# Optimization experiments

Measured on AMD Instinct MI355X. Metric: run time of the kernel, lower is better.

## Reference

```python
import jax, jax.numpy as jnp
import numpy as np

N_S = 50000
N_T = 50000
N = N_S + N_T
D = 128
NEG_SLOPE = 0.2


def gat_conv(x, src, dst, W, a_src, a_dst, n_nodes):
    """PyG GATConv, heads=1, bias=False, add_self_loops=True (loops already appended by caller? no: here)."""
    h = x @ W.T                                   # [N, out]
    loops = jnp.arange(n_nodes, dtype=src.dtype)
    src = jnp.concatenate([src, loops])
    dst = jnp.concatenate([dst, loops])
    a_s = h @ a_src                               # [N]
    a_d = h @ a_dst                               # [N]
    e = jax.nn.leaky_relu(a_s[src] + a_d[dst], NEG_SLOPE)   # [E]
    e_max = jax.ops.segment_max(e, dst, num_segments=n_nodes)
    e = jnp.exp(e - e_max[dst])
    denom = jax.ops.segment_sum(e, dst, num_segments=n_nodes)
    alpha = e / (denom[dst] + 1e-16)
    out = jax.ops.segment_sum(h[src] * alpha[:, None], dst, num_segments=n_nodes)
    return out


def setup_inputs() -> dict:
    key = jax.random.key(0)
    ks = jax.random.split(key, 16)
    E = 500000
    edge_index = jax.random.randint(ks[0], (2, E), 0, N_S, dtype=jnp.int64)
    paper_edge_index = jax.random.randint(ks[1], (2, E), 0, N, dtype=jnp.int64)
    author_edge_index = jax.random.randint(ks[2], (2, E), 0, N, dtype=jnp.int64)
    x_s = jax.random.normal(ks[3], (N_S, D), dtype=jnp.float32)
    x_t = jax.random.normal(ks[4], (N_T, D), dtype=jnp.float32)
    s = 1.0 / np.sqrt(D)
    return {
        "edge_index": edge_index,
        "paper_edge_index": paper_edge_index,
        "author_edge_index": author_edge_index,
        "x_s": x_s,
        "x_t": x_t,
        "Ws": jax.random.normal(ks[5], (D, D), dtype=jnp.float32) * s,
        "bs": jax.random.normal(ks[6], (D,), dtype=jnp.float32) * s,
        "Wt": jax.random.normal(ks[7], (D, D), dtype=jnp.float32) * s,
        "bt": jax.random.normal(ks[8], (D,), dtype=jnp.float32) * s,
        "W1": jax.random.normal(ks[9], (D, D), dtype=jnp.float32) * s,
        "a1s": jax.random.normal(ks[10], (D,), dtype=jnp.float32) * s,
        "a1d": jax.random.normal(ks[11], (D,), dtype=jnp.float32) * s,
        "W2": jax.random.normal(ks[12], (D, D), dtype=jnp.float32) * s,
        "a2s": jax.random.normal(ks[13], (D,), dtype=jnp.float32) * s,
        "a2d": jax.random.normal(ks[14], (D,), dtype=jnp.float32) * s,
    }


def reference(edge_index, paper_edge_index, author_edge_index, x_s, x_t,
              Ws, bs, Wt, bt, W1, a1s, a1d, W2, a2s, a2d):
    # training=None -> no dropout
    x_s = x_s @ Ws.T + bs
    x_t = x_t @ Wt.T + bt
    src = edge_index[0]
    dst = edge_index[1] + N_S  # reindex target nodes into concatenated space
    x = jnp.concatenate([x_s, x_t], axis=0)  # [N, D]

    # conv_1: bipartite edges s->t plus author-author edges
    src1 = jnp.concatenate([src, author_edge_index[0]])
    dst1 = jnp.concatenate([dst, author_edge_index[1]])
    new_x_t = jax.nn.relu(gat_conv(x, src1, dst1, W1, a1s, a1d, N))

    # conv_2: transposed bipartite edges t->s plus paper-paper edges
    src2 = jnp.concatenate([dst, paper_edge_index[0]])
    dst2 = jnp.concatenate([src, paper_edge_index[1]])
    new_x_s = jax.nn.relu(gat_conv(x, src2, dst2, W2, a2s, a2d, N))

    return (new_x_s[:N_S], new_x_t[N_S:])
```

## Files before the change

kernel.cpp:

```cpp
#include <hip/hip_runtime.h>
#include <hip/hip_bf16.h>

#define E0   500000
#define NS   50000
#define DD   128
#define ETOT (2*E0 + NS)

#define OFF_H1   0UL
#define OFF_H2   6400000UL
#define OFF_AS1  12800000UL
#define OFF_AD1  12900000UL
#define OFF_AS2  13000000UL
#define OFF_AD2  13100000UL
#define OFF_DEG1 13200000UL
#define OFF_DEG2 13250000UL
#define OFF_RP1  13300000UL
#define OFF_RP2  13351000UL
#define OFF_CUR1 13402000UL
#define OFF_CUR2 13452000UL
#define OFF_PS   13502000UL
#define OFF_PREF 13502128UL
#define OFF_REC1 13502256UL
#define OFF_REC2 15702256UL

typedef __bf16 bf16x8 __attribute__((ext_vector_type(8)));
typedef float f32x4 __attribute__((ext_vector_type(4)));

__device__ __forceinline__ ushort f2bf(float f) {
    uint b = __float_as_uint(f);
    return (ushort)((b + 0x7FFFu + ((b >> 16) & 1u)) >> 16);
}
__device__ __forceinline__ float bf2f(ushort u) { return __uint_as_float(((uint)u) << 16); }
__device__ __forceinline__ uint pk2(float a, float b) {
    return (uint)f2bf(a) | ((uint)f2bf(b) << 16);
}

__device__ __forceinline__ void stage_w_bf16(ushort* Wl, const float* __restrict__ W, int tid) {
#pragma unroll
    for (int i = 0; i < 8; i++) {
        const int idx = i * 256 + tid;
        const int row = idx >> 4, ch = idx & 15;
        const float4 f0 = *(const float4*)(W + row * DD + ch * 8);
        const float4 f1 = *(const float4*)(W + row * DD + ch * 8 + 4);
        uint4 v = make_uint4(pk2(f0.x, f0.y), pk2(f0.z, f0.w), pk2(f1.x, f1.y), pk2(f1.z, f1.w));
        *(uint4*)((char*)Wl + ((row * 256 + ch * 16) ^ ((row & 7) << 4))) = v;
    }
}

__device__ __forceinline__ void stage_x(ushort* Xl, const float* __restrict__ xin,
                                        int row0, int tid) {
#pragma unroll
    for (int i = 0; i < 4; i++) {
        const int idx = i * 256 + tid;
        const int r = idx >> 4, ch = idx & 15;
        const int gr = row0 + r;
        float4 f0 = make_float4(0.f, 0.f, 0.f, 0.f), f1 = f0;
        if (gr < NS) {
            f0 = *(const float4*)(xin + (size_t)gr * DD + ch * 8);
            f1 = *(const float4*)(xin + (size_t)gr * DD + ch * 8 + 4);
        }
        uint4 v = make_uint4(pk2(f0.x, f0.y), pk2(f0.z, f0.w), pk2(f1.x, f1.y), pk2(f1.z, f1.w));
        *(uint4*)((char*)Xl + ((r * 256 + ch * 16) ^ ((r & 7) << 4))) = v;
    }
}

__device__ __forceinline__ void mfma_phase(const ushort* Wl, const ushort* Xl,
                                           int wrow, int lane, f32x4 acc[8]) {
    const int l15 = lane & 15, q = lane >> 4;
    bf16x8 a[4];
#pragma unroll
    for (int ks = 0; ks < 4; ks++) {
        const int row = wrow + l15;
        const int byte = (row * 256 + (ks * 32 + q * 8) * 2) ^ ((row & 7) << 4);
        a[ks] = *(const bf16x8*)((const char*)Xl + byte);
    }
#pragma unroll
    for (int nt = 0; nt < 8; nt++) {
        const int n = nt * 16 + l15;
#pragma unroll
        for (int ks = 0; ks < 4; ks++) {
            const int byte = (n * 256 + (ks * 32 + q * 8) * 2) ^ ((n & 7) << 4);
            bf16x8 b = *(const bf16x8*)((const char*)Wl + byte);
            acc[nt] = __builtin_amdgcn_mfma_f32_16x16x32_bf16(a[ks], b, acc[nt], 0, 0, 0);
        }
    }
}

__device__ __forceinline__ void epi23(const f32x4 acc[8], int half, int row0, int wrow,
                                      int lane, const float* __restrict__ avs,
                                      const float* __restrict__ avd,
                                      ushort* __restrict__ h,
                                      float* __restrict__ as_, float* __restrict__ ad_) {
    const int l15 = lane & 15, q = lane >> 4;
    float vs[8], vd[8];
#pragma unroll
    for (int nt = 0; nt < 8; nt++) { vs[nt] = avs[nt * 16 + l15]; vd[nt] = avd[nt * 16 + l15]; }
#pragma unroll
    for (int r = 0; r < 4; r++) {
        const int gr = row0 + wrow + q * 4 + r;
        const bool ok = gr < NS;
        const size_t node = (size_t)(half * NS + gr);
        float ps = 0.f, pd = 0.f;
#pragma unroll
        for (int nt = 0; nt < 8; nt++) {
            const float v = acc[nt][r];
            ps += v * vs[nt];
            pd += v * vd[nt];
            if (ok) h[node * DD + nt * 16 + l15] = f2bf(v);
        }
#pragma unroll
        for (int m = 8; m; m >>= 1) { ps += __shfl_xor(ps, m); pd += __shfl_xor(pd, m); }
        if (ok && l15 == 0) { as_[node] = ps; ad_[node] = pd; }
    }
}

__global__ __launch_bounds__(256) void k_gemm(
    const float* __restrict__ xs, const float* __restrict__ xt,
    const float* __restrict__ Ws, const float* __restrict__ bs,
    const float* __restrict__ Wt, const float* __restrict__ bt,
    const float* __restrict__ W1, const float* __restrict__ a1s, const float* __restrict__ a1d,
    const float* __restrict__ W2, const float* __restrict__ a2s, const float* __restrict__ a2d,
    ushort* __restrict__ h1, ushort* __restrict__ h2,
    float* __restrict__ as1, float* __restrict__ ad1,
    float* __restrict__ as2, float* __restrict__ ad2) {
    __shared__ __align__(16) ushort Wl[128 * 128];
    __shared__ __align__(16) ushort Xl[64 * 128];
    const int tid = threadIdx.x;
    const int lane = tid & 63, wv = tid >> 6, wrow = wv * 16;
    const int l15 = lane & 15, q = lane >> 4;
    const int half = blockIdx.y;
    const int row0 = blockIdx.x * 64;
    const float* xin = half ? xt : xs;
    const float* W0  = half ? Wt : Ws;
    const float* b0  = half ? bt : bs;

    stage_w_bf16(Wl, W0, tid);
    stage_x(Xl, xin, row0, tid);
    __syncthreads();

    f32x4 acc[8];
#pragma unroll
    for (int nt = 0; nt < 8; nt++) acc[nt] = 0.f;
    mfma_phase(Wl, Xl, wrow, lane, acc);

#pragma unroll
    for (int nt = 0; nt < 8; nt++) {
        const float bvv = b0[nt * 16 + l15];
#pragma unroll
        for (int r = 0; r < 4; r++) {
            const int row = wrow + q * 4 + r;
            const int byte = (row * 256 + (nt * 16 + l15) * 2) ^ ((row & 7) << 4);
            *(ushort*)((char*)Xl + byte) = f2bf(acc[nt][r] + bvv);
        }
    }
    __syncthreads();
    stage_w_bf16(Wl, W1, tid);
    __syncthreads();

#pragma unroll
    for (int nt = 0; nt < 8; nt++) acc[nt] = 0.f;
    mfma_phase(Wl, Xl, wrow, lane, acc);
    epi23(acc, half, row0, wrow, lane, a1s, a1d, h1, as1, ad1);

    __syncthreads();
    stage_w_bf16(Wl, W2, tid);
    __syncthreads();

#pragma unroll
    for (int nt = 0; nt < 8; nt++) acc[nt] = 0.f;
    mfma_phase(Wl, Xl, wrow, lane, acc);
    epi23(acc, half, row0, wrow, lane, a2s, a2d, h2, as2, ad2);
}

__global__ void k_count_both(const int* __restrict__ ei, const int* __restrict__ pei,
                             const int* __restrict__ aei,
                             int* __restrict__ deg1, int* __restrict__ deg2) {
    const int e = blockIdx.x * 256 + threadIdx.x;
    if (e >= ETOT) return;
    if (e < E0) {
        const int a = ei[e], b = ei[E0 + e];
        atomicAdd(&deg1[b], 1);
        atomicAdd(&deg2[a], 1);
    } else if (e < 2 * E0) {
        const int k = e - E0;
        const int d1 = aei[E0 + k];
        if (d1 >= NS) atomicAdd(&deg1[d1 - NS], 1);
        const int d2 = pei[E0 + k];
        if (d2 < NS) atomicAdd(&deg2[d2], 1);
    } else {
        const int k = e - 2 * E0;
        atomicAdd(&deg1[k], 1);
        atomicAdd(&deg2[k], 1);
    }
}

__device__ __forceinline__ int wave_incl_scan(int x, int lane) {
#pragma unroll
    for (int off = 1; off < 64; off <<= 1) {
        const int v = __shfl_up(x, off);
        if (lane >= off) x += v;
    }
    return x;
}

__device__ __forceinline__ int4 load_deg4(const int* __restrict__ d, int idx) {
    if (idx + 3 < NS) return *(const int4*)(d + idx);
    int4 v = make_int4(0, 0, 0, 0);
    if (idx + 0 < NS) v.x = d[idx + 0];
    if (idx + 1 < NS) v.y = d[idx + 1];
    if (idx + 2 < NS) v.z = d[idx + 2];
    if (idx + 3 < NS) v.w = d[idx + 3];
    return v;
}

__global__ __launch_bounds__(256) void k_scan1(const int* __restrict__ deg,
                                               int* __restrict__ psum) {
    const int conv = blockIdx.y, blk = blockIdx.x, t = threadIdx.x;
    const int* d = deg + conv * NS;
    const int4 v = load_deg4(d, blk * 1024 + t * 4);
    int s = v.x + v.y + v.z + v.w;
#pragma unroll
    for (int m = 32; m; m >>= 1) s += __shfl_xor(s, m);
    __shared__ int wsum[4];
    const int lane = t & 63, wv = t >> 6;
    if (lane == 0) wsum[wv] = s;
    __syncthreads();
    if (t == 0) psum[conv * 64 + blk] = wsum[0] + wsum[1] + wsum[2] + wsum[3];
}

__global__ __launch_bounds__(128) void k_scan2(const int* __restrict__ psum,
                                               int* __restrict__ pref) {
    const int t = threadIdx.x;
    const int w = t >> 6, lane = t & 63;
    const int x = (lane < 49) ? psum[w * 64 + lane] : 0;
    const int incl = wave_incl_scan(x, lane);
    if (lane < 49) pref[w * 64 + lane] = incl - x;
}

__global__ __launch_bounds__(256) void k_scan3(const int* __restrict__ deg,
                                               const int* __restrict__ pref,
                                               int* __restrict__ rp1, int* __restrict__ cur1,
                                               int* __restrict__ rp2, int* __restrict__ cur2) {
    const int conv = blockIdx.y, blk = blockIdx.x, t = threadIdx.x;
    const int* d = deg + conv * NS;
    int* rp  = conv ? rp2  : rp1;
    int* cur = conv ? cur2 : cur1;
    const int idx = blk * 1024 + t * 4;
    const int4 v = load_deg4(d, idx);
    const int tsum = v.x + v.y + v.z + v.w;
    const int lane = t & 63, wv = t >> 6;
    const int incl = wave_incl_scan(tsum, lane);
    __shared__ int wsum[4];
    if (lane == 63) wsum[wv] = incl;
    __syncthreads();
    int woff = 0;
#pragma unroll
    for (int i = 0; i < 4; i++) woff += (i < wv) ? wsum[i] : 0;
    int ex = pref[conv * 64 + blk] + woff + (incl - tsum);
    if (idx + 0 < NS) { rp[idx + 0] = ex; cur[idx + 0] = ex; } ex += v.x;
    if (idx + 1 < NS) { rp[idx + 1] = ex; cur[idx + 1] = ex; } ex += v.y;
    if (idx + 2 < NS) { rp[idx + 2] = ex; cur[idx + 2] = ex; } ex += v.z;
    if (idx + 3 < NS) { rp[idx + 3] = ex; cur[idx + 3] = ex; } ex += v.w;
    if (blk == 48 && t == 0)
        rp[NS] = pref[conv * 64 + 48] + wsum[0] + wsum[1] + wsum[2] + wsum[3];
}

__device__ __forceinline__ float att_ee(float as_v, float ad_v) {
    float v = as_v + ad_v;
    v = v > 0.f ? v : 0.2f * v;
    return __expf(v);
}

__global__ void k_fill_both(const int* __restrict__ ei, const int* __restrict__ pei,
                            const int* __restrict__ aei,
                            const float* __restrict__ as1, const float* __restrict__ ad1,
                            const float* __restrict__ as2, const float* __restrict__ ad2,
                            int* __restrict__ cur1, float2* __restrict__ rec1,
                            int* __restrict__ cur2, float2* __restrict__ rec2) {
    const int e = blockIdx.x * 256 + threadIdx.x;
    if (e >= ETOT) return;
    if (e < E0) {
        const int a = ei[e], b = ei[E0 + e];
        {
            const float ee = att_ee(as1[a], ad1[b + NS]);
            const int pos = atomicAdd(&cur1[b], 1);
            rec1[pos] = make_float2(__int_as_float(a), ee);
        }
        {
            const float ee = att_ee(as2[b + NS], ad2[a]);
            const int pos = atomicAdd(&cur2[a], 1);
            rec2[pos] = make_float2(__int_as_float(b + NS), ee);
        }
    } else if (e < 2 * E0) {
        const int k = e - E0;
        const int s1 = aei[k], d1 = aei[E0 + k];
        if (d1 >= NS) {
            const float ee = att_ee(as1[s1], ad1[d1]);
            const int pos = atomicAdd(&cur1[d1 - NS], 1);
            rec1[pos] = make_float2(__int_as_float(s1), ee);
        }
        const int s2 = pei[k], d2 = pei[E0 + k];
        if (d2 < NS) {
            const float ee = att_ee(as2[s2], ad2[d2]);
            const int pos = atomicAdd(&cur2[d2], 1);
            rec2[pos] = make_float2(__int_as_float(s2), ee);
        }
    } else {
        const int k = e - 2 * E0;
        {
            const float ee = att_ee(as1[NS + k], ad1[NS + k]);
            const int pos = atomicAdd(&cur1[k], 1);
            rec1[pos] = make_float2(__int_as_float(NS + k), ee);
        }
        {
            const float ee = att_ee(as2[k], ad2[k]);
            const int pos = atomicAdd(&cur2[k], 1);
            rec2[pos] = make_float2(__int_as_float(k), ee);
        }
    }
}

__device__ __forceinline__ void fma8(float acc[8], float e, const uint4 q) {
    acc[0] += e * __uint_as_float(q.x << 16);
    acc[1] += e * __uint_as_float(q.x & 0xFFFF0000u);
    acc[2] += e * __uint_as_float(q.y << 16);
    acc[3] += e * __uint_as_float(q.y & 0xFFFF0000u);
    acc[4] += e * __uint_as_float(q.z << 16);
    acc[5] += e * __uint_as_float(q.z & 0xFFFF0000u);
    acc[6] += e * __uint_as_float(q.w << 16);
    acc[7] += e * __uint_as_float(q.w & 0xFFFF0000u);
}

__global__ __launch_bounds__(256) void k_gather(
    const int* __restrict__ rp1, const float2* __restrict__ rec1, const ushort* __restrict__ h1,
    const int* __restrict__ rp2, const float2* __restrict__ rec2, const ushort* __restrict__ h2,
    float* __restrict__ out) {
    const int conv = blockIdx.y;
    const int* rp = conv ? rp2 : rp1;
    const float2* rec = conv ? rec2 : rec1;
    const ushort* h = conv ? h2 : h1;
    float* outb = conv ? out : out + (size_t)NS * DD;
    const int node = blockIdx.x * 4 + (threadIdx.x >> 6);
    const int lane = threadIdx.x & 63;
    const int g = lane >> 4, l16 = lane & 15;
    const int beg = rp[node], end = rp[node + 1];
    float acc[8];
#pragma unroll
    for (int i = 0; i < 8; i++) acc[i] = 0.f;
    float es = 0.f;

    for (int e = beg + g * 4; e < end; e += 16) {
        float w[4];
        int s[4];
#pragma unroll
        for (int u = 0; u < 4; u++) {
            const bool ok = (e + u < end);
            const float2 r = ok ? rec[e + u] : make_float2(0.f, 0.f);
            s[u] = ok ? __float_as_int(r.x) : 0;
            w[u] = r.y;
        }
        uint4 q[4];
#pragma unroll
        for (int u = 0; u < 4; u++)
            q[u] = *(const uint4*)(h + (size_t)s[u] * DD + l16 * 8);
#pragma unroll
        for (int u = 0; u < 4; u++) {
            es += w[u];
            fma8(acc, w[u], q[u]);
        }
    }

#pragma unroll
    for (int i = 0; i < 8; i++) {
        acc[i] += __shfl_xor(acc[i], 16);
        acc[i] += __shfl_xor(acc[i], 32);
    }
    es += __shfl_xor(es, 16);
    es += __shfl_xor(es, 32);

    if (g == 0) {
        const float inv = 1.f / (es + 1e-16f);
        float4 o0, o1;
        o0.x = fmaxf(acc[0] * inv, 0.f);
        o0.y = fmaxf(acc[1] * inv, 0.f);
        o0.z = fmaxf(acc[2] * inv, 0.f);
        o0.w = fmaxf(acc[3] * inv, 0.f);
        o1.x = fmaxf(acc[4] * inv, 0.f);
        o1.y = fmaxf(acc[5] * inv, 0.f);
        o1.z = fmaxf(acc[6] * inv, 0.f);
        o1.w = fmaxf(acc[7] * inv, 0.f);
        *(float4*)(outb + (size_t)node * DD + l16 * 8) = o0;
        *(float4*)(outb + (size_t)node * DD + l16 * 8 + 4) = o1;
    }
}

extern "C" void kernel_launch(void* const* d_in, const int* in_sizes, int n_in,
                              void* d_out, int out_size, void* d_ws, size_t ws_size,
                              hipStream_t stream) {
    const int* ei  = (const int*)d_in[0];
    const int* pei = (const int*)d_in[1];
    const int* aei = (const int*)d_in[2];
    const float* xs  = (const float*)d_in[3];
    const float* xt  = (const float*)d_in[4];
    const float* Ws  = (const float*)d_in[5];
    const float* bs  = (const float*)d_in[6];
    const float* Wt  = (const float*)d_in[7];
    const float* bt  = (const float*)d_in[8];
    const float* W1  = (const float*)d_in[9];
    const float* a1s = (const float*)d_in[10];
    const float* a1d = (const float*)d_in[11];
    const float* W2  = (const float*)d_in[12];
    const float* a2s = (const float*)d_in[13];
    const float* a2d = (const float*)d_in[14];
    float* ws  = (float*)d_ws;
    float* out = (float*)d_out;

    ushort* h1 = (ushort*)(ws + OFF_H1);
    ushort* h2 = (ushort*)(ws + OFF_H2);
    int* deg1 = (int*)(ws + OFF_DEG1);
    int* rp1  = (int*)(ws + OFF_RP1);
    int* rp2  = (int*)(ws + OFF_RP2);
    int* cur1 = (int*)(ws + OFF_CUR1);
    int* cur2 = (int*)(ws + OFF_CUR2);
    int* psum = (int*)(ws + OFF_PS);
    int* pref = (int*)(ws + OFF_PREF);
    float2* rec1 = (float2*)(ws + OFF_REC1);
    float2* rec2 = (float2*)(ws + OFF_REC2);

    hipMemsetAsync(deg1, 0, 2 * NS * sizeof(int), stream);

    k_gemm<<<dim3((NS + 63) / 64, 2), 256, 0, stream>>>(
        xs, xt, Ws, bs, Wt, bt, W1, a1s, a1d, W2, a2s, a2d,
        h1, h2, ws + OFF_AS1, ws + OFF_AD1, ws + OFF_AS2, ws + OFF_AD2);

    const int eb = (ETOT + 255) / 256;
    k_count_both<<<eb, 256, 0, stream>>>(ei, pei, aei, deg1, deg1 + NS);
    k_scan1<<<dim3(49, 2), 256, 0, stream>>>(deg1, psum);
    k_scan2<<<1, 128, 0, stream>>>(psum, pref);
    k_scan3<<<dim3(49, 2), 256, 0, stream>>>(deg1, pref, rp1, cur1, rp2, cur2);
    k_fill_both<<<eb, 256, 0, stream>>>(ei, pei, aei,
                                        ws + OFF_AS1, ws + OFF_AD1, ws + OFF_AS2, ws + OFF_AD2,
                                        cur1, rec1, cur2, rec2);
    k_gather<<<dim3(NS / 4, 2), 256, 0, stream>>>(rp1, rec1, h1, rp2, rec2, h2, out);
}
```

Measured before the change: 366.5 us.

## Record atomic slots at count time and fuse CSR fill into GEMM launch

The degree-count pass now stores each edge's atomic slot, so the CSR fill becomes a plain scatter with no second round of atomics and no cursor arrays. That scatter is merged into the GEMM kernel as extra blocks, letting memory-bound edge work overlap the MFMA-bound projection blocks in a single launch. The per-edge attention exponent moves into the gather kernel, computed from as/ad lookups, so records shrink to 4-byte source indices. The cost is an extra slot array written and read, one more random as[] load per edge inside the gather, and a fused kernel whose edge blocks are forced to the GEMM block's shared-memory and launch-bounds footprint.

```diff
diff --git a/kernel.cpp b/kernel.cpp
--- a/kernel.cpp
+++ b/kernel.cpp
@@ -6,22 +6,25 @@
 #define DD   128
 #define ETOT (2*E0 + NS)
 
-#define OFF_H1   0UL
-#define OFF_H2   6400000UL
-#define OFF_AS1  12800000UL
-#define OFF_AD1  12900000UL
-#define OFF_AS2  13000000UL
-#define OFF_AD2  13100000UL
-#define OFF_DEG1 13200000UL
-#define OFF_DEG2 13250000UL
-#define OFF_RP1  13300000UL
-#define OFF_RP2  13351000UL
-#define OFF_CUR1 13402000UL
-#define OFF_CUR2 13452000UL
-#define OFF_PS   13502000UL
-#define OFF_PREF 13502128UL
-#define OFF_REC1 13502256UL
-#define OFF_REC2 15702256UL
+#define GEMM_BLOCKS 1564
+#define EDGE_BLOCKS 4102
+
+#define OFF_H1    0UL
+#define OFF_H2    6400000UL
+#define OFF_AS1   12800000UL
+#define OFF_AD1   12900000UL
+#define OFF_AS2   13000000UL
+#define OFF_AD2   13100000UL
+#define OFF_DEG1  13200000UL
+#define OFF_DEG2  13250000UL
+#define OFF_RP1   13300000UL
+#define OFF_RP2   13351000UL
+#define OFF_PS    13402000UL
+#define OFF_PREF  13402128UL
+#define OFF_SLOT1 13402256UL
+#define OFF_SLOT2 14452256UL
+#define OFF_REC1  15502256UL
+#define OFF_REC2  16552256UL
 
 typedef __bf16 bf16x8 __attribute__((ext_vector_type(8)));
 typedef float f32x4 __attribute__((ext_vector_type(4)));
@@ -30,7 +33,6 @@
     uint b = __float_as_uint(f);
     return (ushort)((b + 0x7FFFu + ((b >> 16) & 1u)) >> 16);
 }
-__device__ __forceinline__ float bf2f(ushort u) { return __uint_as_float(((uint)u) << 16); }
 __device__ __forceinline__ uint pk2(float a, float b) {
     return (uint)f2bf(a) | ((uint)f2bf(b) << 16);
 }
@@ -114,7 +116,7 @@
     }
 }
 
-__global__ __launch_bounds__(256) void k_gemm(
+__global__ __launch_bounds__(256) void k_fat(
     const float* __restrict__ xs, const float* __restrict__ xt,
     const float* __restrict__ Ws, const float* __restrict__ bs,
     const float* __restrict__ Wt, const float* __restrict__ bt,
@@ -122,14 +124,41 @@
     const float* __restrict__ W2, const float* __restrict__ a2s, const float* __restrict__ a2d,
     ushort* __restrict__ h1, ushort* __restrict__ h2,
     float* __restrict__ as1, float* __restrict__ ad1,
-    float* __restrict__ as2, float* __restrict__ ad2) {
+    float* __restrict__ as2, float* __restrict__ ad2,
+    const int* __restrict__ ei, const int* __restrict__ pei, const int* __restrict__ aei,
+    const int* __restrict__ rp1, const int* __restrict__ rp2,
+    const int* __restrict__ slot1, const int* __restrict__ slot2,
+    int* __restrict__ rec1, int* __restrict__ rec2) {
     __shared__ __align__(16) ushort Wl[128 * 128];
     __shared__ __align__(16) ushort Xl[64 * 128];
+    const int bid = blockIdx.x;
     const int tid = threadIdx.x;
+
+    if (bid >= GEMM_BLOCKS) {
+        const int e = (bid - GEMM_BLOCKS) * 256 + tid;
+        if (e >= ETOT) return;
+        if (e < E0) {
+            const int a = ei[e], b = ei[E0 + e];
+            rec1[rp1[b] + slot1[e]] = a;
+            rec2[rp2[a] + slot2[e]] = b + NS;
+        } else if (e < 2 * E0) {
+            const int k = e - E0;
+            const int s1 = aei[k], d1 = aei[E0 + k];
+            if (d1 >= NS) rec1[rp1[d1 - NS] + slot1[e]] = s1;
+            const int s2 = pei[k], d2 = pei[E0 + k];
+            if (d2 < NS) rec2[rp2[d2] + slot2[e]] = s2;
+        } else {
+            const int k = e - 2 * E0;
+            rec1[rp1[k] + slot1[e]] = NS + k;
+            rec2[rp2[k] + slot2[e]] = k;
+        }
+        return;
+    }
+
     const int lane = tid & 63, wv = tid >> 6, wrow = wv * 16;
     const int l15 = lane & 15, q = lane >> 4;
-    const int half = blockIdx.y;
-    const int row0 = blockIdx.x * 64;
+    const int half = (bid >= 782) ? 1 : 0;
+    const int row0 = (bid - half * 782) * 64;
     const float* xin = half ? xt : xs;
     const float* W0  = half ? Wt : Ws;
     const float* b0  = half ? bt : bs;
@@ -174,23 +203,24 @@
 
 __global__ void k_count_both(const int* __restrict__ ei, const int* __restrict__ pei,
                              const int* __restrict__ aei,
-                             int* __restrict__ deg1, int* __restrict__ deg2) {
+                             int* __restrict__ deg1, int* __restrict__ deg2,
+                             int* __restrict__ slot1, int* __restrict__ slot2) {
     const int e = blockIdx.x * 256 + threadIdx.x;
     if (e >= ETOT) return;
     if (e < E0) {
         const int a = ei[e], b = ei[E0 + e];
-        atomicAdd(&deg1[b], 1);
-        atomicAdd(&deg2[a], 1);
+        slot1[e] = atomicAdd(&deg1[b], 1);
+        slot2[e] = atomicAdd(&deg2[a], 1);
     } else if (e < 2 * E0) {
         const int k = e - E0;
         const int d1 = aei[E0 + k];
-        if (d1 >= NS) atomicAdd(&deg1[d1 - NS], 1);
+        if (d1 >= NS) slot1[e] = atomicAdd(&deg1[d1 - NS], 1);
         const int d2 = pei[E0 + k];
-        if (d2 < NS) atomicAdd(&deg2[d2], 1);
+        if (d2 < NS) slot2[e] = atomicAdd(&deg2[d2], 1);
     } else {
         const int k = e - 2 * E0;
-        atomicAdd(&deg1[k], 1);
-        atomicAdd(&deg2[k], 1);
+        slot1[e] = atomicAdd(&deg1[k], 1);
+        slot2[e] = atomicAdd(&deg2[k], 1);
     }
 }
 
@@ -239,12 +269,10 @@
 
 __global__ __launch_bounds__(256) void k_scan3(const int* __restrict__ deg,
                                                const int* __restrict__ pref,
-                                               int* __restrict__ rp1, int* __restrict__ cur1,
-                                               int* __restrict__ rp2, int* __restrict__ cur2) {
+                                               int* __restrict__ rp1, int* __restrict__ rp2) {
     const int conv = blockIdx.y, blk = blockIdx.x, t = threadIdx.x;
     const int* d = deg + conv * NS;
-    int* rp  = conv ? rp2  : rp1;
-    int* cur = conv ? cur2 : cur1;
+    int* rp = conv ? rp2 : rp1;
     const int idx = blk * 1024 + t * 4;
     const int4 v = load_deg4(d, idx);
     const int tsum = v.x + v.y + v.z + v.w;
@@ -257,67 +285,12 @@
 #pragma unroll
     for (int i = 0; i < 4; i++) woff += (i < wv) ? wsum[i] : 0;
     int ex = pref[conv * 64 + blk] + woff + (incl - tsum);
-    if (idx + 0 < NS) { rp[idx + 0] = ex; cur[idx + 0] = ex; } ex += v.x;
-    if (idx + 1 < NS) { rp[idx + 1] = ex; cur[idx + 1] = ex; } ex += v.y;
-    if (idx + 2 < NS) { rp[idx + 2] = ex; cur[idx + 2] = ex; } ex += v.z;
-    if (idx + 3 < NS) { rp[idx + 3] = ex; cur[idx + 3] = ex; } ex += v.w;
+    if (idx + 0 < NS) rp[idx + 0] = ex; ex += v.x;
+    if (idx + 1 < NS) rp[idx + 1] = ex; ex += v.y;
+    if (idx + 2 < NS) rp[idx + 2] = ex; ex += v.z;
+    if (idx + 3 < NS) rp[idx + 3] = ex; ex += v.w;
     if (blk == 48 && t == 0)
         rp[NS] = pref[conv * 64 + 48] + wsum[0] + wsum[1] + wsum[2] + wsum[3];
-}
-
-__device__ __forceinline__ float att_ee(float as_v, float ad_v) {
-    float v = as_v + ad_v;
-    v = v > 0.f ? v : 0.2f * v;
-    return __expf(v);
-}
-
-__global__ void k_fill_both(const int* __restrict__ ei, const int* __restrict__ pei,
-                            const int* __restrict__ aei,
-                            const float* __restrict__ as1, const float* __restrict__ ad1,
-                            const float* __restrict__ as2, const float* __restrict__ ad2,
-                            int* __restrict__ cur1, float2* __restrict__ rec1,
-                            int* __restrict__ cur2, float2* __restrict__ rec2) {
-    const int e = blockIdx.x * 256 + threadIdx.x;
-    if (e >= ETOT) return;
-    if (e < E0) {
-        const int a = ei[e], b = ei[E0 + e];
-        {
-            const float ee = att_ee(as1[a], ad1[b + NS]);
-            const int pos = atomicAdd(&cur1[b], 1);
-            rec1[pos] = make_float2(__int_as_float(a), ee);
-        }
-        {
-            const float ee = att_ee(as2[b + NS], ad2[a]);
-            const int pos = atomicAdd(&cur2[a], 1);
-            rec2[pos] = make_float2(__int_as_float(b + NS), ee);
-        }
-    } else if (e < 2 * E0) {
-        const int k = e - E0;
-        const int s1 = aei[k], d1 = aei[E0 + k];
-        if (d1 >= NS) {
-            const float ee = att_ee(as1[s1], ad1[d1]);
-            const int pos = atomicAdd(&cur1[d1 - NS], 1);
-            rec1[pos] = make_float2(__int_as_float(s1), ee);
-        }
-        const int s2 = pei[k], d2 = pei[E0 + k];
-        if (d2 < NS) {
-            const float ee = att_ee(as2[s2], ad2[d2]);
-            const int pos = atomicAdd(&cur2[d2], 1);
-            rec2[pos] = make_float2(__int_as_float(s2), ee);
-        }
-    } else {
-        const int k = e - 2 * E0;
-        {
-            const float ee = att_ee(as1[NS + k], ad1[NS + k]);
-            const int pos = atomicAdd(&cur1[k], 1);
-            rec1[pos] = make_float2(__int_as_float(NS + k), ee);
-        }
-        {
-            const float ee = att_ee(as2[k], ad2[k]);
-            const int pos = atomicAdd(&cur2[k], 1);
-            rec2[pos] = make_float2(__int_as_float(k), ee);
-        }
-    }
 }
 
 __device__ __forceinline__ void fma8(float acc[8], float e, const uint4 q) {
@@ -332,37 +305,45 @@
 }
 
 __global__ __launch_bounds__(256) void k_gather(
-    const int* __restrict__ rp1, const float2* __restrict__ rec1, const ushort* __restrict__ h1,
-    const int* __restrict__ rp2, const float2* __restrict__ rec2, const ushort* __restrict__ h2,
+    const int* __restrict__ rp1, const int* __restrict__ rec1, const ushort* __restrict__ h1,
+    const float* __restrict__ as1, const float* __restrict__ ad1,
+    const int* __restrict__ rp2, const int* __restrict__ rec2, const ushort* __restrict__ h2,
+    const float* __restrict__ as2, const float* __restrict__ ad2,
     float* __restrict__ out) {
     const int conv = blockIdx.y;
     const int* rp = conv ? rp2 : rp1;
-    const float2* rec = conv ? rec2 : rec1;
+    const int* rec = conv ? rec2 : rec1;
     const ushort* h = conv ? h2 : h1;
+    const float* as_ = conv ? as2 : as1;
+    const float* ad_ = conv ? ad2 : ad1;
     float* outb = conv ? out : out + (size_t)NS * DD;
     const int node = blockIdx.x * 4 + (threadIdx.x >> 6);
+    const int gd = conv ? node : node + NS;
     const int lane = threadIdx.x & 63;
     const int g = lane >> 4, l16 = lane & 15;
     const int beg = rp[node], end = rp[node + 1];
+    const float adv = ad_[gd];
     float acc[8];
 #pragma unroll
     for (int i = 0; i < 8; i++) acc[i] = 0.f;
     float es = 0.f;
 
-    for (int e = beg + g * 4; e < end; e += 16) {
-        float w[4];
+    for (int e0 = beg + g * 4; e0 < end; e0 += 16) {
         int s[4];
 #pragma unroll
-        for (int u = 0; u < 4; u++) {
-            const bool ok = (e + u < end);
-            const float2 r = ok ? rec[e + u] : make_float2(0.f, 0.f);
-            s[u] = ok ? __float_as_int(r.x) : 0;
-            w[u] = r.y;
-        }
+        for (int u = 0; u < 4; u++)
+            s[u] = (e0 + u < end) ? rec[e0 + u] : 0;
         uint4 q[4];
 #pragma unroll
         for (int u = 0; u < 4; u++)
             q[u] = *(const uint4*)(h + (size_t)s[u] * DD + l16 * 8);
+        float w[4];
+#pragma unroll
+        for (int u = 0; u < 4; u++) {
+            float ev = as_[s[u]] + adv;
+            ev = ev > 0.f ? ev : 0.2f * ev;
+            w[u] = (e0 + u < end) ? __expf(ev) : 0.f;
+        }
 #pragma unroll
         for (int u = 0; u < 4; u++) {
             es += w[u];
@@ -417,29 +398,32 @@
 
     ushort* h1 = (ushort*)(ws + OFF_H1);
     ushort* h2 = (ushort*)(ws + OFF_H2);
-    int* deg1 = (int*)(ws + OFF_DEG1);
-    int* rp1  = (int*)(ws + OFF_RP1);
-    int* rp2  = (int*)(ws + OFF_RP2);
-    int* cur1 = (int*)(ws + OFF_CUR1);
-    int* cur2 = (int*)(ws + OFF_CUR2);
-    int* psum = (int*)(ws + OFF_PS);
-    int* pref = (int*)(ws + OFF_PREF);
-    float2* rec1 = (float2*)(ws + OFF_REC1);
-    float2* rec2 = (float2*)(ws + OFF_REC2);
+    float* as1 = ws + OFF_AS1;
+    float* ad1 = ws + OFF_AD1;
+    float* as2 = ws + OFF_AS2;
+    float* ad2 = ws + OFF_AD2;
+    int* deg1  = (int*)(ws + OFF_DEG1);
+    int* rp1   = (int*)(ws + OFF_RP1);
+    int* rp2   = (int*)(ws + OFF_RP2);
+    int* psum  = (int*)(ws + OFF_PS);
+    int* pref  = (int*)(ws + OFF_PREF);
+    int* slot1 = (int*)(ws + OFF_SLOT1);
+    int* slot2 = (int*)(ws + OFF_SLOT2);
+    int* rec1  = (int*)(ws + OFF_REC1);
+    int* rec2  = (int*)(ws + OFF_REC2);
 
     hipMemsetAsync(deg1, 0, 2 * NS * sizeof(int), stream);
 
-    k_gemm<<<dim3((NS + 63) / 64, 2), 256, 0, stream>>>(
-        xs, xt, Ws, bs, Wt, bt, W1, a1s, a1d, W2, a2s, a2d,
-        h1, h2, ws + OFF_AS1, ws + OFF_AD1, ws + OFF_AS2, ws + OFF_AD2);
-
-    const int eb = (ETOT + 255) / 256;
-    k_count_both<<<eb, 256, 0, stream>>>(ei, pei, aei, deg1, deg1 + NS);
+    k_count_both<<<EDGE_BLOCKS, 256, 0, stream>>>(ei, pei, aei, deg1, deg1 + NS, slot1, slot2);
     k_scan1<<<dim3(49, 2), 256, 0, stream>>>(deg1, psum);
     k_scan2<<<1, 128, 0, stream>>>(psum, pref);
-    k_scan3<<<dim3(49, 2), 256, 0, stream>>>(deg1, pref, rp1, cur1, rp2, cur2);
-    k_fill_both<<<eb, 256, 0, stream>>>(ei, pei, aei,
-                                        ws + OFF_AS1, ws + OFF_AD1, ws + OFF_AS2, ws + OFF_AD2,
-                                        cur1, rec1, cur2, rec2);
-    k_gather<<<dim3(NS / 4, 2), 256, 0, stream>>>(rp1, rec1, h1, rp2, rec2, h2, out);
-}
+    k_scan3<<<dim3(49, 2), 256, 0, stream>>>(deg1, pref, rp1, rp2);
+
+    k_fat<<<GEMM_BLOCKS + EDGE_BLOCKS, 256, 0, stream>>>(
+        xs, xt, Ws, bs, Wt, bt, W1, a1s, a1d, W2, a2s, a2d,
+        h1, h2, as1, ad1, as2, ad2,
+        ei, pei, aei, rp1, rp2, slot1, slot2, rec1, rec2);
+
+    k_gather<<<dim3(NS / 4, 2), 256, 0, stream>>>(
+        rp1, rec1, h1, as1, ad1, rp2, rec2, h2, as2, ad2, out);
+}
```

Result: faster. 319.8 us (-12.7%).
